# Optimization experiments

Measured on AMD Instinct MI355X. Metric: run time of the kernel, lower is better.

The kernel has to match this reference:

```python
import jax, jax.numpy as jnp
import numpy as np

# Architecture constants (match init_kwargs)
L, M, K, P, G = 3, 4096, 2, 4, 4
NUM_IN, NUM_OUT, B = 8192, 1000, 2048
F = 6          # number of combinact activation functions
EPS_BN = 1e-5  # BatchNorm1d eps
EPS = 1e-12    # numeric safety for sqrt


def setup_inputs() -> dict:
    key = jax.random.key(0)
    ks = jax.random.split(key, 8)
    x = jax.random.normal(ks[0], (B, NUM_IN), jnp.float32)
    # shuffle maps: perm 0 is identity (the un-permuted copy), perms 1..P-1 random
    rng = np.random.default_rng(0)
    perms = np.stack([
        np.stack([np.arange(M)] + [rng.permutation(M) for _ in range(P - 1)])
        for _ in range(L)
    ]).astype(np.int32)  # (L, P, M)
    cin_g = NUM_IN // G  # per-group input width (curr stays 8192 every layer)
    W = jax.random.normal(ks[1], (L, G, M // G, cin_g), jnp.float32) / np.sqrt(cin_g)
    b = jax.random.normal(ks[2], (L, G, M // G), jnp.float32) * 0.01
    gamma = jnp.ones((L, M), jnp.float32)
    beta = jnp.zeros((L, M), jnp.float32)
    # original inits alpha_primes to zeros; small random gives non-degenerate mixing
    alpha = jax.random.normal(ks[3], (L, P, F), jnp.float32) * 0.1
    d_last = (M // K) * P
    W_out = jax.random.normal(ks[4], (NUM_OUT, d_last), jnp.float32) / np.sqrt(d_last)
    b_out = jnp.zeros((NUM_OUT,), jnp.float32)
    return {"x": x, "perms": jnp.asarray(perms), "W": W, "b": b,
            "gamma": gamma, "beta": beta, "alpha": alpha,
            "W_out": W_out, "b_out": b_out}


def _combinact(z, alpha_l):
    # z: (B, clusters, K, P) -> (B, clusters, P); per-perm softmax mixing
    sig = jax.nn.sigmoid(z)
    pr = jnp.prod(z, axis=2)
    acts = jnp.stack([
        jnp.max(z, axis=2),                          # max
        jnp.sign(pr) * jnp.sqrt(jnp.abs(pr) + EPS),  # signed geomean (k=2)
        z[:, :, 0, :] * jnp.prod(sig, axis=2),       # swish-k
        jnp.sqrt(jnp.sum(z * z, axis=2) + EPS),      # l2
        jnp.max(jnp.abs(z), axis=2),                 # linf
        jax.nn.logsumexp(z, axis=2),                 # lse
    ], axis=0)  # (F, B, clusters, P)
    w = jax.nn.softmax(alpha_l, axis=-1)  # (P, F)
    return jnp.einsum('fbcp,pf->bcp', acts, w)


def _forward(x, perms, W, b, gamma, beta, alpha, W_out, b_out):
    h = x
    for l in range(L):
        C = h.shape[1]
        # grouped small linears: (B, C/G, G) x (G, M/G, C/G) -> (B, M/G, G) -> (B, M)
        hr = h.reshape(B, C // G, G)
        y = jnp.einsum('bcg,gmc->bmg', hr, W[l]) + b[l].T[None]
        y = y.reshape(B, M)
        # BatchNorm1d (training mode, biased batch var)
        mu = jnp.mean(y, axis=0)
        var = jnp.mean((y - mu) ** 2, axis=0)
        y = (y - mu) * jax.lax.rsqrt(var + EPS_BN) * gamma[l] + beta[l]
        # p permuted copies, reshape into clusters of k
        zc = y[:, perms[l]]                                   # (B, P, M) gather
        z = jnp.transpose(zc, (0, 2, 1)).reshape(B, M // K, K, P)
        a = _combinact(z, alpha[l])                           # (B, M/K, P)
        h = jnp.transpose(a, (0, 2, 1)).reshape(B, (M // K) * P)
    return h @ W_out.T + b_out


def reference(x, perms, W, b, gamma, beta, alpha, W_out, b_out):
    return _forward(x, perms, W, b, gamma, beta, alpha, W_out, b_out)
```

## Files before the change

### kernel.cpp

```cpp
#include <hip/hip_runtime.h>
#include <math.h>

#define Lnum 3
#define Mdim 4096
#define Pdim 4
#define Gdim 4
#define NIN 8192
#define NOUT 1000
#define Bdim 2048
#define Fdim 6
#define CIN 2048
#define MG 1024
#define CH 2048
#define DNEXT 8192
#define NRCHUNK (Bdim / 128)

typedef short bf16x8 __attribute__((ext_vector_type(8)));
typedef float f32x4 __attribute__((ext_vector_type(4)));

__device__ __forceinline__ short f2bf(float f) {
    union { float f; unsigned u; } v; v.f = f;
    unsigned u = v.u;
    unsigned r = (u + 0x7fffu + ((u >> 16) & 1u)) >> 16;
    return (short)r;
}
__device__ __forceinline__ float bf2f(short h) {
    union { unsigned u; float f; } x;
    x.u = ((unsigned)(unsigned short)h) << 16;
    return x.f;
}

__global__ __launch_bounds__(256) void convert_f32_bf16(
    const float* __restrict__ src, short* __restrict__ dst, int n8)
{
    int i = blockIdx.x * 256 + threadIdx.x;
    if (i >= n8) return;
    const float4* s = (const float4*)src + (size_t)i * 2;
    float4 v0 = s[0], v1 = s[1];
    bf16x8 o;
    o[0] = f2bf(v0.x); o[1] = f2bf(v0.y); o[2] = f2bf(v0.z); o[3] = f2bf(v0.w);
    o[4] = f2bf(v1.x); o[5] = f2bf(v1.y); o[6] = f2bf(v1.z); o[7] = f2bf(v1.w);
    *((bf16x8*)dst + i) = o;
}

__global__ __launch_bounds__(256) void convert_wo(
    const float* __restrict__ src, short* __restrict__ dst)
{
    int i = blockIdx.x * 256 + threadIdx.x;
    int row = i >> 10;
    bf16x8 o;
    if (row < NOUT) {
        const float4* s = (const float4*)(src + (size_t)row * DNEXT + (i & 1023) * 8);
        float4 v0 = s[0], v1 = s[1];
        o[0] = f2bf(v0.x); o[1] = f2bf(v0.y); o[2] = f2bf(v0.z); o[3] = f2bf(v0.w);
        o[4] = f2bf(v1.x); o[5] = f2bf(v1.y); o[6] = f2bf(v1.z); o[7] = f2bf(v1.w);
    } else {
        for (int j = 0; j < 8; ++j) o[j] = 0;
    }
    *((bf16x8*)dst + i) = o;
}

__global__ __launch_bounds__(256) void x_to_grouped(
    const float* __restrict__ x, short* __restrict__ hg)
{
    const int c = blockIdx.x * 256 + threadIdx.x;
    const int b = blockIdx.y;
    float4 v = *(const float4*)(x + (size_t)b * NIN + 4 * c);
    const size_t plane = (size_t)Bdim * CIN;
    hg[0 * plane + (size_t)b * CIN + c] = f2bf(v.x);
    hg[1 * plane + (size_t)b * CIN + c] = f2bf(v.y);
    hg[2 * plane + (size_t)b * CIN + c] = f2bf(v.z);
    hg[3 * plane + (size_t)b * CIN + c] = f2bf(v.w);
}

__global__ __launch_bounds__(256) void remap_perms(
    const int* __restrict__ perm, int* __restrict__ perm_g, int n)
{
    int i = blockIdx.x * 256 + threadIdx.x;
    if (i >= n) return;
    int j  = perm[i];
    int jg = ((j & 3) << 10) | (j >> 2);
    perm_g[i] = jg ^ ((jg >> 3) & 3);
}

template<int BN_T, int NWARP, bool STATS, typename CT>
__global__ __launch_bounds__(NWARP * 64) void gemm_mfma(
    const short* __restrict__ A0, size_t aZ, int lda,
    const short* __restrict__ B0, size_t bZ, int ldb,
    const float* __restrict__ bias0, size_t biasZ,
    CT* __restrict__ C0, size_t cZ,
    int K, int ldc, int nbound,
    float* __restrict__ psum, float* __restrict__ psumsq, int sgz)
{
    constexpr int NT   = NWARP * 64;
    constexpr int WCN  = NWARP / 2;
    constexpr int WCOL = BN_T / WCN;
    constexpr int FN   = WCOL / 16;

    const int nx = gridDim.x, ny = gridDim.y;
    const int nwg = nx * ny * gridDim.z;
    const int lin = blockIdx.x + nx * (blockIdx.y + ny * blockIdx.z);
    int swz = (lin & 7) * (nwg >> 3) + (lin >> 3);
    const int bx = swz % nx; swz /= nx;
    const int by = swz % ny;
    const int g  = swz / ny;

    const short* A  = A0 + aZ * g;
    const short* Bm = B0 + bZ * g;
    CT* C = C0 + cZ * g;

    const int n0 = bx * BN_T;
    const int b0 = by * 128;

    __shared__ short As[2][128 * 64];
    __shared__ short Bs[2][BN_T * 64];

    const int tid  = threadIdx.x;
    const int w    = tid >> 6;
    const int lane = tid & 63;
    const int wr = w / WCN, wc = w % WCN;

    f32x4 acc[4][FN];
#pragma unroll
    for (int m = 0; m < 4; ++m)
#pragma unroll
        for (int n = 0; n < FN; ++n) acc[m][n] = (f32x4)0.f;

    auto stage = [&](int buf, int k0) {
#pragma unroll
        for (int idx = tid; idx < 128 * 8; idx += NT) {
            const int r = idx >> 3, slot = idx & 7;
            const int gs = slot ^ (r & 7);
            const short* ga = A + (size_t)(b0 + r) * lda + k0 + gs * 8;
            __builtin_amdgcn_global_load_lds(
                (const __attribute__((address_space(1))) void*)ga,
                (__attribute__((address_space(3))) void*)(&As[buf][idx * 8]), 16, 0, 0);
        }
#pragma unroll
        for (int idx = tid; idx < BN_T * 8; idx += NT) {
            const int r = idx >> 3, slot = idx & 7;
            const int gs = slot ^ (r & 7);
            const short* gb = Bm + (size_t)(n0 + r) * ldb + k0 + gs * 8;
            __builtin_amdgcn_global_load_lds(
                (const __attribute__((address_space(1))) void*)gb,
                (__attribute__((address_space(3))) void*)(&Bs[buf][idx * 8]), 16, 0, 0);
        }
    };

    const int fr15 = lane & 15;
    const int fq   = lane >> 4;

    auto compute = [&](int buf) {
#pragma unroll
        for (int kk = 0; kk < 2; ++kk) {
            bf16x8 af[4], bff[FN];
            const int kob = kk * 64 + fq * 16;
#pragma unroll
            for (int m = 0; m < 4; ++m) {
                const int r  = wr * 64 + m * 16 + fr15;
                const int sw = kob ^ ((r & 7) << 4);
                af[m] = *(const bf16x8*)(&As[buf][r * 64 + (sw >> 1)]);
            }
#pragma unroll
            for (int n = 0; n < FN; ++n) {
                const int r  = wc * WCOL + n * 16 + fr15;
                const int sw = kob ^ ((r & 7) << 4);
                bff[n] = *(const bf16x8*)(&Bs[buf][r * 64 + (sw >> 1)]);
            }
#pragma unroll
            for (int m = 0; m < 4; ++m)
#pragma unroll
                for (int n = 0; n < FN; ++n)
                    acc[m][n] = __builtin_amdgcn_mfma_f32_16x16x32_bf16(af[m], bff[n], acc[m][n], 0, 0, 0);
        }
    };

    stage(0, 0);

    const int nt = K >> 6;
    int p = 0;
    for (int t = 0; t < nt - 1; ++t) {
        stage(p ^ 1, (t + 1) << 6);
        asm volatile("s_waitcnt vmcnt(4)" ::: "memory");
        __builtin_amdgcn_s_barrier();
        asm volatile("" ::: "memory");
        compute(p);
        asm volatile("" ::: "memory");
        __builtin_amdgcn_s_barrier();
        p ^= 1;
    }
    asm volatile("s_waitcnt vmcnt(0)" ::: "memory");
    __builtin_amdgcn_s_barrier();
    asm volatile("" ::: "memory");
    compute(p);

    float s[FN], ss[FN];
#pragma unroll
    for (int n = 0; n < FN; ++n) { s[n] = 0.f; ss[n] = 0.f; }

#pragma unroll
    for (int m = 0; m < 4; ++m) {
#pragma unroll
        for (int n = 0; n < FN; ++n) {
#pragma unroll
            for (int j = 0; j < 4; ++j) {
                const int row = b0 + wr * 64 + m * 16 + fq * 4 + j;
                const int col = n0 + wc * WCOL + n * 16 + fr15;
                if (col < nbound) {
                    float v = acc[m][n][j];
                    if (bias0) v += bias0[biasZ * g + col];
                    C[(size_t)row * ldc + col] = (CT)(sizeof(CT) == 2 ? (CT)f2bf(v) : (CT)v);
                    if (STATS) { s[n] += v; ss[n] += v * v; }
                }
            }
        }
    }

    if (STATS) {
        __syncthreads();
        float* sum_lds = (float*)&As[0][0];
        float* ssq_lds = sum_lds + BN_T * 8;
        const int slot = wr * 4 + fq;
#pragma unroll
        for (int n = 0; n < FN; ++n) {
            const int cl = wc * WCOL + n * 16 + fr15;
            sum_lds[cl * 8 + slot] = s[n];
            ssq_lds[cl * 8 + slot] = ss[n];
        }
        __syncthreads();
        for (int cl = tid; cl < BN_T; cl += NT) {
            float a = 0.f, b = 0.f;
#pragma unroll
            for (int q = 0; q < 8; ++q) {
                a += sum_lds[cl * 8 + q];
                b += ssq_lds[cl * 8 + q];
            }
            const size_t o = (size_t)by * Mdim + g * sgz + n0 + cl;
            psum[o]   = a;
            psumsq[o] = b;
        }
    }
}

__global__ __launch_bounds__(256) void reduce_out(
    const float* __restrict__ part, const float* __restrict__ bo,
    float* __restrict__ out)
{
    const int n = blockIdx.x * 256 + threadIdx.x;
    const int b = blockIdx.y;
    if (n >= NOUT) return;
    const size_t S = (size_t)Bdim * 1024;
    const size_t i = (size_t)b * 1024 + n;
    out[(size_t)b * NOUT + n] =
        part[i] + part[S + i] + part[2 * S + i] + part[3 * S + i] + bo[n];
}

__global__ __launch_bounds__(256) void bn_finalize(
    const float* __restrict__ psum, const float* __restrict__ psumsq,
    const float* __restrict__ gamma, const float* __restrict__ beta,
    float* __restrict__ scale, float* __restrict__ shift)
{
    const int jg = blockIdx.x * 256 + threadIdx.x;
    if (jg >= Mdim) return;
    const int j = ((jg & 1023) << 2) | (jg >> 10);
    float s = 0.f, ss = 0.f;
    for (int r = 0; r < NRCHUNK; ++r) {
        s  += psum[r * Mdim + jg];
        ss += psumsq[r * Mdim + jg];
    }
    const float mu  = s * (1.f / Bdim);
    const float var = ss * (1.f / Bdim) - mu * mu;
    const float sc  = gamma[j] * rsqrtf(var + 1e-5f);
    scale[jg] = sc;
    shift[jg] = beta[j] - mu * sc;
}

__global__ void alpha_softmax(const float* __restrict__ alpha, float* __restrict__ wsm)
{
    const int idx = threadIdx.x;
    if (idx >= Lnum * Pdim) return;
    const float* a = alpha + idx * Fdim;
    float mx = a[0];
#pragma unroll
    for (int f = 1; f < Fdim; ++f) mx = fmaxf(mx, a[f]);
    float e[Fdim]; float s = 0.f;
#pragma unroll
    for (int f = 0; f < Fdim; ++f) { e[f] = __expf(a[f] - mx); s += e[f]; }
    const float inv = 1.f / s;
#pragma unroll
    for (int f = 0; f < Fdim; ++f) wsm[idx * Fdim + f] = e[f] * inv;
}

template<int MODE>
__global__ __launch_bounds__(512) void combinact_kernel(
    const short* __restrict__ Y, const float* __restrict__ scale,
    const float* __restrict__ shift, const int* __restrict__ perm,
    const float* __restrict__ wsm, short* __restrict__ out)
{
    __shared__ f32x4 zE[Mdim];
    const int b0  = blockIdx.x * 2;
    const int tid = threadIdx.x;
    const float L2E = 1.44269504f;
    const float LN2 = 0.69314718f;

    {
        const int i8   = tid;
        const int base = i8 * 8;
        const bf16x8 v0 = *((const bf16x8*)(Y + (size_t)(b0 + 0) * Mdim) + i8);
        const bf16x8 v1 = *((const bf16x8*)(Y + (size_t)(b0 + 1) * Mdim) + i8);
        const int xr = i8 & 3;
#pragma unroll
        for (int jj = 0; jj < 8; ++jj) {
            const float sc = scale[base + jj];
            const float sh = shift[base + jj];
            f32x4 t;
            t[0] = bf2f(v0[jj]) * sc + sh;
            t[1] = bf2f(v1[jj]) * sc + sh;
            t[2] = __builtin_amdgcn_exp2f(L2E * t[0]);
            t[3] = __builtin_amdgcn_exp2f(L2E * t[1]);
            zE[base + (jj ^ xr)] = t;
        }
    }
    __syncthreads();

    float wv[Pdim][Fdim];
#pragma unroll
    for (int p = 0; p < Pdim; ++p)
#pragma unroll
        for (int f = 0; f < Fdim; ++f) wv[p][f] = wsm[p * Fdim + f];

    const size_t plane = (size_t)Bdim * CIN;

#pragma unroll
    for (int k = 0; k < 4; ++k) {
        const int idx = k * 512 + tid;
        int c, g = 0, q = 0;
        if (MODE == 0) { g = idx >> 9; q = idx & 511; c = q * 4 + g; }
        else           { c = idx; }

#pragma unroll
        for (int p = 0; p < Pdim; ++p) {
            const int2 jj = *(const int2*)(perm + p * Mdim + 2 * c);
            const f32x4 c0 = zE[jj.x];
            const f32x4 c1 = zE[jj.y];

#pragma unroll
            for (int r = 0; r < 2; ++r) {
                const float z0 = c0[r],     z1 = c1[r];
                const float E0 = c0[2 + r], E1 = c1[2 + r];

                const float mx = fmaxf(z0, z1);
                const float pr = z0 * z1;
                const float a1 = copysignf(__builtin_amdgcn_sqrtf(fabsf(pr) + 1e-12f), pr);
                const float a2 = z0 * E0 * E1 *
                                 __builtin_amdgcn_rcpf((1.f + E0) * (1.f + E1));
                const float a3 = __builtin_amdgcn_sqrtf(z0 * z0 + z1 * z1 + 1e-12f);
                const float a4 = fmaxf(fabsf(z0), fabsf(z1));
                const float a5 = LN2 * __builtin_amdgcn_logf(E0 + E1);

                const float v = wv[p][0] * mx + wv[p][1] * a1 + wv[p][2] * a2 +
                                wv[p][3] * a3 + wv[p][4] * a4 + wv[p][5] * a5;

                if (MODE == 0)
                    out[g * plane + (size_t)(b0 + r) * CIN + p * 512 + q] = f2bf(v);
                else
                    out[(size_t)(b0 + r) * DNEXT + p * CH + c] = f2bf(v);
            }
        }
    }
}

extern "C" void kernel_launch(void* const* d_in, const int* in_sizes, int n_in,
                              void* d_out, int out_size, void* d_ws, size_t ws_size,
                              hipStream_t stream)
{
    const float* x     = (const float*)d_in[0];
    const int*   perms = (const int*)  d_in[1];
    const float* W     = (const float*)d_in[2];
    const float* bvec  = (const float*)d_in[3];
    const float* gamma = (const float*)d_in[4];
    const float* beta  = (const float*)d_in[5];
    const float* alpha = (const float*)d_in[6];
    const float* Wo    = (const float*)d_in[7];
    const float* bo    = (const float*)d_in[8];
    float* out = (float*)d_out;

    char* ws = (char*)d_ws;
    short* y      = (short*)ws;
    short* hg     = y + (size_t)Bdim * Mdim;
    short* Wlb3   = hg + (size_t)Gdim * Bdim * CIN;
    short* Wob    = Wlb3 + (size_t)Lnum * Gdim * MG * CIN;
    float* psum   = (float*)(Wob + (size_t)1024 * DNEXT);
    float* psumsq = psum + (size_t)NRCHUNK * Mdim;
    float* scale  = psumsq + (size_t)NRCHUNK * Mdim;
    float* shift  = scale + Mdim;
    float* wsm    = shift + Mdim;
    int*   perm_g = (int*)(wsm + Lnum * Pdim * Fdim);

    short* hflat = hg;
    float* part  = (float*)Wlb3;

    alpha_softmax<<<1, 64, 0, stream>>>(alpha, wsm);
    remap_perms<<<(Lnum * Pdim * Mdim) / 256, 256, 0, stream>>>(
        perms, perm_g, Lnum * Pdim * Mdim);
    convert_f32_bf16<<<(Lnum * Gdim * MG * CIN / 8) / 256, 256, 0, stream>>>(
        W, Wlb3, Lnum * Gdim * MG * CIN / 8);
    convert_wo<<<(1024 * 1024) / 256, 256, 0, stream>>>(Wo, Wob);
    x_to_grouped<<<dim3(CIN / 256, Bdim), 256, 0, stream>>>(x, hg);

    const size_t planeA = (size_t)Bdim * CIN;
    const size_t planeB = (size_t)MG * CIN;

    for (int l = 0; l < Lnum; ++l) {
        dim3 gg(MG / 128, Bdim / 128, Gdim);
        gemm_mfma<128, 8, true, short><<<gg, 512, 0, stream>>>(
            hg, planeA, CIN, Wlb3 + (size_t)l * Gdim * MG * CIN, planeB, CIN,
            bvec + (size_t)l * Gdim * MG, (size_t)MG,
            y, (size_t)MG,
            CIN, Mdim, MG,
            psum, psumsq, MG);

        bn_finalize<<<Mdim / 256, 256, 0, stream>>>(
            psum, psumsq, gamma + (size_t)l * Mdim, beta + (size_t)l * Mdim, scale, shift);

        if (l < Lnum - 1)
            combinact_kernel<0><<<Bdim / 2, 512, 0, stream>>>(
                y, scale, shift, perm_g + (size_t)l * Pdim * Mdim, wsm + l * Pdim * Fdim, hg);
        else
            combinact_kernel<1><<<Bdim / 2, 512, 0, stream>>>(
                y, scale, shift, perm_g + (size_t)l * Pdim * Mdim, wsm + l * Pdim * Fdim, hflat);
    }

    dim3 go(1024 / 128, Bdim / 128, 4);
    gemm_mfma<128, 8, false, float><<<go, 512, 0, stream>>>(
        hflat, (size_t)2048, DNEXT, Wob, (size_t)2048, DNEXT,
        nullptr, 0,
        part, (size_t)Bdim * 1024,
        2048, 1024, 1024,
        nullptr, nullptr, 0);

    dim3 gr(4, Bdim);
    reduce_out<<<gr, 256, 0, stream>>>(part, bo, out);
}
```

Measured before the change: 298.3 us.

## Simplify GEMM to single-buffered 4-warp tiles and fuse prep kernels into one launch

Replaces the double-buffered 8-warp GEMM with BK=64 by a single-buffered 4-warp version with BK=32 and plain __syncthreads between load and compute. The five preprocessing kernels (weight conversion, input regrouping, perm remap, alpha softmax) are merged into one launch to cut launch overhead. The GEMM change removes the overlap of global-to-LDS loads with MFMA work and halves the k-step depth, which risks exposing memory latency in the dominant matmuls. Lower LDS use may allow more resident blocks.

```diff
diff --git a/kernel.cpp b/kernel.cpp
--- a/kernel.cpp
+++ b/kernel.cpp
@@ -30,61 +30,70 @@
     return x.f;
 }
 
-__global__ __launch_bounds__(256) void convert_f32_bf16(
-    const float* __restrict__ src, short* __restrict__ dst, int n8)
-{
-    int i = blockIdx.x * 256 + threadIdx.x;
-    if (i >= n8) return;
-    const float4* s = (const float4*)src + (size_t)i * 2;
-    float4 v0 = s[0], v1 = s[1];
-    bf16x8 o;
-    o[0] = f2bf(v0.x); o[1] = f2bf(v0.y); o[2] = f2bf(v0.z); o[3] = f2bf(v0.w);
-    o[4] = f2bf(v1.x); o[5] = f2bf(v1.y); o[6] = f2bf(v1.z); o[7] = f2bf(v1.w);
-    *((bf16x8*)dst + i) = o;
-}
-
-__global__ __launch_bounds__(256) void convert_wo(
-    const float* __restrict__ src, short* __restrict__ dst)
-{
-    int i = blockIdx.x * 256 + threadIdx.x;
-    int row = i >> 10;
-    bf16x8 o;
-    if (row < NOUT) {
-        const float4* s = (const float4*)(src + (size_t)row * DNEXT + (i & 1023) * 8);
+__global__ __launch_bounds__(256) void prep_all(
+    const float* __restrict__ W, short* __restrict__ Wlb3,
+    const float* __restrict__ Wo, short* __restrict__ Wob,
+    const float* __restrict__ x, short* __restrict__ hg,
+    const int* __restrict__ perms, int* __restrict__ perm_g,
+    const float* __restrict__ alpha, float* __restrict__ wsm)
+{
+    const int blk = blockIdx.x;
+    const int tid = threadIdx.x;
+
+    if (blk < 12288) {
+        const int i = blk * 256 + tid;
+        const float4* s = (const float4*)W + (size_t)i * 2;
         float4 v0 = s[0], v1 = s[1];
+        bf16x8 o;
         o[0] = f2bf(v0.x); o[1] = f2bf(v0.y); o[2] = f2bf(v0.z); o[3] = f2bf(v0.w);
         o[4] = f2bf(v1.x); o[5] = f2bf(v1.y); o[6] = f2bf(v1.z); o[7] = f2bf(v1.w);
+        *((bf16x8*)Wlb3 + i) = o;
+    } else if (blk < 16384) {
+        const int i = (blk - 12288) * 256 + tid;
+        const int row = i >> 10;
+        bf16x8 o;
+        if (row < NOUT) {
+            const float4* s = (const float4*)(Wo + (size_t)row * DNEXT + (i & 1023) * 8);
+            float4 v0 = s[0], v1 = s[1];
+            o[0] = f2bf(v0.x); o[1] = f2bf(v0.y); o[2] = f2bf(v0.z); o[3] = f2bf(v0.w);
+            o[4] = f2bf(v1.x); o[5] = f2bf(v1.y); o[6] = f2bf(v1.z); o[7] = f2bf(v1.w);
+        } else {
+            for (int j = 0; j < 8; ++j) o[j] = 0;
+        }
+        *((bf16x8*)Wob + i) = o;
+    } else if (blk < 32768) {
+        const int idx = (blk - 16384) * 256 + tid;
+        const int b = idx >> 11;
+        const int c = idx & 2047;
+        float4 v = *(const float4*)(x + (size_t)b * NIN + 4 * c);
+        const size_t plane = (size_t)Bdim * CIN;
+        hg[0 * plane + (size_t)b * CIN + c] = f2bf(v.x);
+        hg[1 * plane + (size_t)b * CIN + c] = f2bf(v.y);
+        hg[2 * plane + (size_t)b * CIN + c] = f2bf(v.z);
+        hg[3 * plane + (size_t)b * CIN + c] = f2bf(v.w);
+    } else if (blk < 32960) {
+        const int i = (blk - 32768) * 256 + tid;
+        int j  = perms[i];
+        int jg = ((j & 3) << 10) | (j >> 2);
+        perm_g[i] = jg ^ ((jg >> 3) & 3);
     } else {
-        for (int j = 0; j < 8; ++j) o[j] = 0;
-    }
-    *((bf16x8*)dst + i) = o;
-}
-
-__global__ __launch_bounds__(256) void x_to_grouped(
-    const float* __restrict__ x, short* __restrict__ hg)
-{
-    const int c = blockIdx.x * 256 + threadIdx.x;
-    const int b = blockIdx.y;
-    float4 v = *(const float4*)(x + (size_t)b * NIN + 4 * c);
-    const size_t plane = (size_t)Bdim * CIN;
-    hg[0 * plane + (size_t)b * CIN + c] = f2bf(v.x);
-    hg[1 * plane + (size_t)b * CIN + c] = f2bf(v.y);
-    hg[2 * plane + (size_t)b * CIN + c] = f2bf(v.z);
-    hg[3 * plane + (size_t)b * CIN + c] = f2bf(v.w);
-}
-
-__global__ __launch_bounds__(256) void remap_perms(
-    const int* __restrict__ perm, int* __restrict__ perm_g, int n)
-{
-    int i = blockIdx.x * 256 + threadIdx.x;
-    if (i >= n) return;
-    int j  = perm[i];
-    int jg = ((j & 3) << 10) | (j >> 2);
-    perm_g[i] = jg ^ ((jg >> 3) & 3);
-}
-
-template<int BN_T, int NWARP, bool STATS, typename CT>
-__global__ __launch_bounds__(NWARP * 64) void gemm_mfma(
+        if (tid < Lnum * Pdim) {
+            const float* a = alpha + tid * Fdim;
+            float mx = a[0];
+#pragma unroll
+            for (int f = 1; f < Fdim; ++f) mx = fmaxf(mx, a[f]);
+            float e[Fdim]; float s = 0.f;
+#pragma unroll
+            for (int f = 0; f < Fdim; ++f) { e[f] = __expf(a[f] - mx); s += e[f]; }
+            const float inv = 1.f / s;
+#pragma unroll
+            for (int f = 0; f < Fdim; ++f) wsm[tid * Fdim + f] = e[f] * inv;
+        }
+    }
+}
+
+template<bool STATS, typename CT>
+__global__ __launch_bounds__(256) void gemm_mfma(
     const short* __restrict__ A0, size_t aZ, int lda,
     const short* __restrict__ B0, size_t bZ, int ldb,
     const float* __restrict__ bias0, size_t biasZ,
@@ -92,11 +101,6 @@
     int K, int ldc, int nbound,
     float* __restrict__ psum, float* __restrict__ psumsq, int sgz)
 {
-    constexpr int NT   = NWARP * 64;
-    constexpr int WCN  = NWARP / 2;
-    constexpr int WCOL = BN_T / WCN;
-    constexpr int FN   = WCOL / 16;
-
     const int nx = gridDim.x, ny = gridDim.y;
     const int nwg = nx * ny * gridDim.z;
     const int lin = blockIdx.x + nx * (blockIdx.y + ny * blockIdx.z);
@@ -109,103 +113,90 @@
     const short* Bm = B0 + bZ * g;
     CT* C = C0 + cZ * g;
 
-    const int n0 = bx * BN_T;
+    const int n0 = bx * 128;
     const int b0 = by * 128;
 
-    __shared__ short As[2][128 * 64];
-    __shared__ short Bs[2][BN_T * 64];
+    __shared__ short As[128 * 32];
+    __shared__ short Bs[128 * 32];
 
     const int tid  = threadIdx.x;
     const int w    = tid >> 6;
     const int lane = tid & 63;
-    const int wr = w / WCN, wc = w % WCN;
-
-    f32x4 acc[4][FN];
+    const int wr = w >> 1, wc = w & 1;
+
+    f32x4 acc[4][4];
 #pragma unroll
     for (int m = 0; m < 4; ++m)
 #pragma unroll
-        for (int n = 0; n < FN; ++n) acc[m][n] = (f32x4)0.f;
-
-    auto stage = [&](int buf, int k0) {
-#pragma unroll
-        for (int idx = tid; idx < 128 * 8; idx += NT) {
-            const int r = idx >> 3, slot = idx & 7;
-            const int gs = slot ^ (r & 7);
+        for (int n = 0; n < 4; ++n) acc[m][n] = (f32x4)0.f;
+
+    const int fr15 = lane & 15;
+    const int fq   = lane >> 4;
+
+    auto stage = [&](int k0) {
+#pragma unroll
+        for (int q = 0; q < 2; ++q) {
+            const int idx = tid + q * 256;
+            const int r = idx >> 2, slot = idx & 3;
+            const int gs = slot ^ (r & 3);
             const short* ga = A + (size_t)(b0 + r) * lda + k0 + gs * 8;
             __builtin_amdgcn_global_load_lds(
                 (const __attribute__((address_space(1))) void*)ga,
-                (__attribute__((address_space(3))) void*)(&As[buf][idx * 8]), 16, 0, 0);
-        }
-#pragma unroll
-        for (int idx = tid; idx < BN_T * 8; idx += NT) {
-            const int r = idx >> 3, slot = idx & 7;
-            const int gs = slot ^ (r & 7);
+                (__attribute__((address_space(3))) void*)(&As[idx * 8]), 16, 0, 0);
+        }
+#pragma unroll
+        for (int q = 0; q < 2; ++q) {
+            const int idx = tid + q * 256;
+            const int r = idx >> 2, slot = idx & 3;
+            const int gs = slot ^ (r & 3);
             const short* gb = Bm + (size_t)(n0 + r) * ldb + k0 + gs * 8;
             __builtin_amdgcn_global_load_lds(
                 (const __attribute__((address_space(1))) void*)gb,
-                (__attribute__((address_space(3))) void*)(&Bs[buf][idx * 8]), 16, 0, 0);
+                (__attribute__((address_space(3))) void*)(&Bs[idx * 8]), 16, 0, 0);
         }
     };
 
-    const int fr15 = lane & 15;
-    const int fq   = lane >> 4;
-
-    auto compute = [&](int buf) {
-#pragma unroll
-        for (int kk = 0; kk < 2; ++kk) {
-            bf16x8 af[4], bff[FN];
-            const int kob = kk * 64 + fq * 16;
-#pragma unroll
-            for (int m = 0; m < 4; ++m) {
-                const int r  = wr * 64 + m * 16 + fr15;
-                const int sw = kob ^ ((r & 7) << 4);
-                af[m] = *(const bf16x8*)(&As[buf][r * 64 + (sw >> 1)]);
-            }
-#pragma unroll
-            for (int n = 0; n < FN; ++n) {
-                const int r  = wc * WCOL + n * 16 + fr15;
-                const int sw = kob ^ ((r & 7) << 4);
-                bff[n] = *(const bf16x8*)(&Bs[buf][r * 64 + (sw >> 1)]);
-            }
-#pragma unroll
-            for (int m = 0; m < 4; ++m)
-#pragma unroll
-                for (int n = 0; n < FN; ++n)
-                    acc[m][n] = __builtin_amdgcn_mfma_f32_16x16x32_bf16(af[m], bff[n], acc[m][n], 0, 0, 0);
-        }
+    auto compute = [&]() {
+        bf16x8 af[4], bff[4];
+#pragma unroll
+        for (int m = 0; m < 4; ++m) {
+            const int r = wr * 64 + m * 16 + fr15;
+            const int s = fq ^ (r & 3);
+            af[m] = *(const bf16x8*)(&As[r * 32 + s * 8]);
+        }
+#pragma unroll
+        for (int n = 0; n < 4; ++n) {
+            const int r = wc * 64 + n * 16 + fr15;
+            const int s = fq ^ (r & 3);
+            bff[n] = *(const bf16x8*)(&Bs[r * 32 + s * 8]);
+        }
+#pragma unroll
+        for (int m = 0; m < 4; ++m)
+#pragma unroll
+            for (int n = 0; n < 4; ++n)
+                acc[m][n] = __builtin_amdgcn_mfma_f32_16x16x32_bf16(af[m], bff[n], acc[m][n], 0, 0, 0);
     };
 
-    stage(0, 0);
-
-    const int nt = K >> 6;
-    int p = 0;
-    for (int t = 0; t < nt - 1; ++t) {
-        stage(p ^ 1, (t + 1) << 6);
-        asm volatile("s_waitcnt vmcnt(4)" ::: "memory");
-        __builtin_amdgcn_s_barrier();
-        asm volatile("" ::: "memory");
-        compute(p);
-        asm volatile("" ::: "memory");
-        __builtin_amdgcn_s_barrier();
-        p ^= 1;
-    }
-    asm volatile("s_waitcnt vmcnt(0)" ::: "memory");
-    __builtin_amdgcn_s_barrier();
-    asm volatile("" ::: "memory");
-    compute(p);
-
-    float s[FN], ss[FN];
-#pragma unroll
-    for (int n = 0; n < FN; ++n) { s[n] = 0.f; ss[n] = 0.f; }
+    const int nt = K >> 5;
+    for (int t = 0; t < nt; ++t) {
+        stage(t << 5);
+        __syncthreads();
+        compute();
+        __syncthreads();
+    }
+
+    float s[4], ss[4];
+#pragma unroll
+    for (int n = 0; n < 4; ++n) { s[n] = 0.f; ss[n] = 0.f; }
 
 #pragma unroll
     for (int m = 0; m < 4; ++m) {
 #pragma unroll
-        for (int n = 0; n < FN; ++n) {
+        for (int n = 0; n < 4; ++n) {
 #pragma unroll
             for (int j = 0; j < 4; ++j) {
                 const int row = b0 + wr * 64 + m * 16 + fq * 4 + j;
-                const int col = n0 + wc * WCOL + n * 16 + fr15;
+                const int col = n0 + wc * 64 + n * 16 + fr15;
                 if (col < nbound) {
                     float v = acc[m][n][j];
                     if (bias0) v += bias0[biasZ * g + col];
@@ -218,17 +209,17 @@
 
     if (STATS) {
         __syncthreads();
-        float* sum_lds = (float*)&As[0][0];
-        float* ssq_lds = sum_lds + BN_T * 8;
+        float* sum_lds = (float*)&As[0];
+        float* ssq_lds = sum_lds + 128 * 8;
         const int slot = wr * 4 + fq;
 #pragma unroll
-        for (int n = 0; n < FN; ++n) {
-            const int cl = wc * WCOL + n * 16 + fr15;
+        for (int n = 0; n < 4; ++n) {
+            const int cl = wc * 64 + n * 16 + fr15;
             sum_lds[cl * 8 + slot] = s[n];
             ssq_lds[cl * 8 + slot] = ss[n];
         }
         __syncthreads();
-        for (int cl = tid; cl < BN_T; cl += NT) {
+        for (int cl = tid; cl < 128; cl += 256) {
             float a = 0.f, b = 0.f;
 #pragma unroll
             for (int q = 0; q < 8; ++q) {
@@ -273,22 +264,6 @@
     const float sc  = gamma[j] * rsqrtf(var + 1e-5f);
     scale[jg] = sc;
     shift[jg] = beta[j] - mu * sc;
-}
-
-__global__ void alpha_softmax(const float* __restrict__ alpha, float* __restrict__ wsm)
-{
-    const int idx = threadIdx.x;
-    if (idx >= Lnum * Pdim) return;
-    const float* a = alpha + idx * Fdim;
-    float mx = a[0];
-#pragma unroll
-    for (int f = 1; f < Fdim; ++f) mx = fmaxf(mx, a[f]);
-    float e[Fdim]; float s = 0.f;
-#pragma unroll
-    for (int f = 0; f < Fdim; ++f) { e[f] = __expf(a[f] - mx); s += e[f]; }
-    const float inv = 1.f / s;
-#pragma unroll
-    for (int f = 0; f < Fdim; ++f) wsm[idx * Fdim + f] = e[f] * inv;
 }
 
 template<int MODE>
@@ -400,20 +375,15 @@
     short* hflat = hg;
     float* part  = (float*)Wlb3;
 
-    alpha_softmax<<<1, 64, 0, stream>>>(alpha, wsm);
-    remap_perms<<<(Lnum * Pdim * Mdim) / 256, 256, 0, stream>>>(
-        perms, perm_g, Lnum * Pdim * Mdim);
-    convert_f32_bf16<<<(Lnum * Gdim * MG * CIN / 8) / 256, 256, 0, stream>>>(
-        W, Wlb3, Lnum * Gdim * MG * CIN / 8);
-    convert_wo<<<(1024 * 1024) / 256, 256, 0, stream>>>(Wo, Wob);
-    x_to_grouped<<<dim3(CIN / 256, Bdim), 256, 0, stream>>>(x, hg);
+    prep_all<<<32961, 256, 0, stream>>>(
+        W, Wlb3, Wo, Wob, x, hg, perms, perm_g, alpha, wsm);
 
     const size_t planeA = (size_t)Bdim * CIN;
     const size_t planeB = (size_t)MG * CIN;
 
     for (int l = 0; l < Lnum; ++l) {
         dim3 gg(MG / 128, Bdim / 128, Gdim);
-        gemm_mfma<128, 8, true, short><<<gg, 512, 0, stream>>>(
+        gemm_mfma<true, short><<<gg, 256, 0, stream>>>(
             hg, planeA, CIN, Wlb3 + (size_t)l * Gdim * MG * CIN, planeB, CIN,
             bvec + (size_t)l * Gdim * MG, (size_t)MG,
             y, (size_t)MG,
@@ -432,7 +402,7 @@
     }
 
     dim3 go(1024 / 128, Bdim / 128, 4);
-    gemm_mfma<128, 8, false, float><<<go, 512, 0, stream>>>(
+    gemm_mfma<false, float><<<go, 256, 0, stream>>>(
         hflat, (size_t)2048, DNEXT, Wob, (size_t)2048, DNEXT,
         nullptr, 0,
         part, (size_t)Bdim * 1024,
```

After: 371.2 us. 1.24x slower.
